# Kernel tuning notes

Measured on AMD Instinct MI355X. Metric: run time of the kernel, lower is better.

Reference implementation:

```python
import jax, jax.numpy as jnp
import numpy as np

D_MODEL = 768
N_HEADS = 12
D_K = D_MODEL // N_HEADS
NEG_INF = -1e9


def setup_inputs() -> dict:
    key = jax.random.key(0)
    ks = jax.random.split(key, 7)
    B, S = 4, 2048
    x = jax.random.normal(ks[0], (B, S, D_MODEL), dtype=jnp.float32)
    # causal mask, broadcastable to [B, H, S, S]
    mask = jnp.tril(jnp.ones((S, S), dtype=bool))[None, None, :, :]
    scale = 1.0 / np.sqrt(D_MODEL)
    Wq = jax.random.normal(ks[1], (D_MODEL, D_MODEL), dtype=jnp.float32) * scale
    bq = jnp.zeros((D_MODEL,), dtype=jnp.float32)
    Wk = jax.random.normal(ks[2], (D_MODEL, D_MODEL), dtype=jnp.float32) * scale
    bk = jnp.zeros((D_MODEL,), dtype=jnp.float32)
    Wv = jax.random.normal(ks[3], (D_MODEL, D_MODEL), dtype=jnp.float32) * scale
    bv = jnp.zeros((D_MODEL,), dtype=jnp.float32)
    return {"x": x, "mask": mask, "Wq": Wq, "bq": bq, "Wk": Wk, "bk": bk, "Wv": Wv, "bv": bv}


def reference(x, mask, Wq, bq, Wk, bk, Wv, bv):
    B, S, _ = x.shape
    # projections (torch Linear: y = x @ W.T + b)
    q = (x @ Wq.T + bq).reshape(B, S, N_HEADS, D_K)
    k = (x @ Wk.T + bk).reshape(B, S, N_HEADS, D_K)
    v = (x @ Wv.T + bv).reshape(B, S, N_HEADS, D_K)
    # scores: [B, H, S, S]
    scores = jnp.einsum("bqhd,bkhd->bhqk", q, k) / jnp.sqrt(jnp.float32(D_K))
    scores = jnp.where(mask, scores, NEG_INF)
    probs = jax.nn.softmax(scores, axis=-1)
    # attention: [B, H, S, D_K] -> [B, S, d_model]
    attn = jnp.einsum("bhqk,bkhd->bqhd", probs, v).reshape(B, S, D_MODEL)
    return attn
```

## Files before the change

kernel.cpp:

```cpp
#include <hip/hip_runtime.h>
#include <math.h>


#define S_LEN 2048
#define BATCH 4
#define HEADS 12
#define DM 768
#define DK 64
#define BH (BATCH*HEADS)
#define MROWS (BATCH*S_LEN)
#define QSCALE 0.1803368801111244f

typedef __attribute__((ext_vector_type(8))) short short8;
typedef __attribute__((ext_vector_type(4))) float floatx4;
typedef __attribute__((address_space(3))) unsigned char lds_byte;
typedef __attribute__((address_space(1))) const unsigned char glob_byte;

__device__ __forceinline__ unsigned short f2bf(float f) {
  union { float f; unsigned int u; } a; a.f = f;
  unsigned int u = a.u;
  return (unsigned short)((u + 0x7fffu + ((u >> 16) & 1u)) >> 16);
}
__device__ __forceinline__ unsigned short f2bf_rtz(float f) {
  union { float f; unsigned int u; } a; a.f = f;
  return (unsigned short)(a.u >> 16);
}

__global__ void cast_f32_bf16(const float* __restrict__ src,
                              unsigned short* __restrict__ dst, int n) {
  int i = (blockIdx.x * blockDim.x + threadIdx.x) * 4;
  if (i < n) {
    float4 v = *(const float4*)(src + i);
    ushort4 o;
    o.x = f2bf(v.x); o.y = f2bf(v.y); o.z = f2bf(v.z); o.w = f2bf(v.w);
    *(ushort4*)(dst + i) = o;
  }
}

__global__ void cast_w3(const float* __restrict__ w0, const float* __restrict__ w1,
                        const float* __restrict__ w2, unsigned short* __restrict__ dst,
                        int n) {
  const float* src = (blockIdx.y == 0) ? w0 : (blockIdx.y == 1) ? w1 : w2;
  int i = (blockIdx.x * blockDim.x + threadIdx.x) * 4;
  if (i < n) {
    float4 v = *(const float4*)(src + i);
    ushort4 o;
    o.x = f2bf(v.x); o.y = f2bf(v.y); o.z = f2bf(v.z); o.w = f2bf(v.w);
    *(ushort4*)(dst + (size_t)blockIdx.y * n + i) = o;
  }
}

__global__ __launch_bounds__(256) void qkv_gemm(
    const unsigned short* __restrict__ xb,
    const unsigned short* __restrict__ wb,
    const float* __restrict__ bq, const float* __restrict__ bk,
    const float* __restrict__ bv,
    unsigned short* __restrict__ qo,
    unsigned short* __restrict__ ko,
    unsigned short* __restrict__ vto) {
  __shared__ unsigned short a_lds[2 * 128 * 32];
  __shared__ unsigned short b_lds[2 * 128 * 32];
  const int mat = blockIdx.z;
  const int tid = threadIdx.x;
  const int wave = tid >> 6, lane = tid & 63, quad = lane >> 4, ln = lane & 15;
  const int wm = wave & 1, wn = wave >> 1;
  const int m_blk = blockIdx.x * 128, n_blk = blockIdx.y * 128;
  const unsigned short* w = wb + (size_t)mat * DM * DM;
  const int srow_i[2] = { (0 * 256 + wave * 64 + lane) >> 2,
                          (1 * 256 + wave * 64 + lane) >> 2 };
  const int sq = (lane & 3) * 8;

  const floatx4 fz = {0.f, 0.f, 0.f, 0.f};
  floatx4 acc[4][4];
#pragma unroll
  for (int mg = 0; mg < 4; mg++)
#pragma unroll
    for (int c = 0; c < 4; c++) acc[mg][c] = fz;

  for (int k0 = 0; k0 < DM; k0 += 64) {
#pragma unroll
    for (int p = 0; p < 2; p++)
#pragma unroll
      for (int i = 0; i < 2; i++) {
        const int cbase = i * 256 + wave * 64;
        const int row = srow_i[i];
        __builtin_amdgcn_global_load_lds(
            (glob_byte*)(xb + (size_t)(m_blk + row) * DM + k0 + p * 32 + sq),
            (lds_byte*)(a_lds + p * 4096 + cbase * 8), 16, 0, 0);
        __builtin_amdgcn_global_load_lds(
            (glob_byte*)(w + (size_t)(n_blk + row) * DM + k0 + p * 32 + sq),
            (lds_byte*)(b_lds + p * 4096 + cbase * 8), 16, 0, 0);
      }
    __syncthreads();

    short8 af[4][2], bf[4][2];
#pragma unroll
    for (int mg = 0; mg < 4; mg++)
#pragma unroll
      for (int p = 0; p < 2; p++)
        af[mg][p] = *(const short8*)(a_lds + p * 4096 + (wm * 64 + mg * 16 + ln) * 32 + quad * 8);
#pragma unroll
    for (int c = 0; c < 4; c++)
#pragma unroll
      for (int p = 0; p < 2; p++)
        bf[c][p] = *(const short8*)(b_lds + p * 4096 + (wn * 64 + c * 16 + ln) * 32 + quad * 8);
#pragma unroll
    for (int mg = 0; mg < 4; mg++)
#pragma unroll
      for (int c = 0; c < 4; c++) {
        acc[mg][c] = __builtin_amdgcn_mfma_f32_16x16x32_bf16(af[mg][0], bf[c][0], acc[mg][c], 0, 0, 0);
        acc[mg][c] = __builtin_amdgcn_mfma_f32_16x16x32_bf16(af[mg][1], bf[c][1], acc[mg][c], 0, 0, 0);
      }
    __syncthreads();
  }

  const float* bias = (mat == 0) ? bq : (mat == 1) ? bk : bv;
  const float oscale = (mat == 0) ? QSCALE : 1.0f;
  const int m_base = m_blk + wm * 64, n_base = n_blk + wn * 64;
#pragma unroll
  for (int mg = 0; mg < 4; mg++)
#pragma unroll
    for (int c = 0; c < 4; c++) {
      int gn = n_base + c * 16 + ln;
      int hd = gn >> 6, d = gn & 63;
      float bias_v = bias[gn] * oscale;
      int gm0 = m_base + mg * 16 + quad * 4;
      int bb = gm0 >> 11, s0 = gm0 & (S_LEN - 1);
      if (mat == 2) {
        ushort4 pk;
        pk.x = f2bf(acc[mg][c][0] + bias_v);
        pk.y = f2bf(acc[mg][c][1] + bias_v);
        pk.z = f2bf(acc[mg][c][2] + bias_v);
        pk.w = f2bf(acc[mg][c][3] + bias_v);
        *(ushort4*)(vto + (((size_t)(bb * HEADS + hd)) * DK + d) * S_LEN + s0) = pk;
      } else {
        unsigned short* dst = (mat == 0 ? qo : ko) +
            (((size_t)(bb * HEADS + hd)) * S_LEN + s0) * DK + d;
#pragma unroll
        for (int r = 0; r < 4; r++)
          dst[(size_t)r * DK] = f2bf(acc[mg][c][r] * oscale + bias_v);
      }
    }
}

__global__ __launch_bounds__(128) void flash_attn(
    const unsigned short* __restrict__ q,
    const unsigned short* __restrict__ k,
    const unsigned short* __restrict__ vt,
    float* __restrict__ out) {
  __shared__ unsigned short p_lds[2][32 * 64];
  const int id = blockIdx.x;
  const int bh = id % BH;
  const int qt = (S_LEN / 64 - 1) - (id / BH);
  const int q0 = qt * 64;
  const int tid = threadIdx.x;
  const int wave = tid >> 6, lane = tid & 63, quad = lane >> 4, ln = lane & 15;
  unsigned short* pl = p_lds[wave];
  const unsigned short* qp = q  + (size_t)bh * S_LEN * DK;
  const unsigned short* kp = k  + (size_t)bh * S_LEN * DK;
  const unsigned short* vp = vt + (size_t)bh * DK * S_LEN;
  const int qr_base = q0 + wave * 32;
  const floatx4 fz = {0.f, 0.f, 0.f, 0.f};

  unsigned short* wp[4];
#pragma unroll
  for (int kg = 0; kg < 4; kg++)
    wp[kg] = pl + quad * 256 + (((((kg ^ quad) & 3) << 1) | (ln >> 3)) * 8) + (ln & 7);
  const unsigned short* rp[2];
#pragma unroll
  for (int ss = 0; ss < 2; ss++)
    rp[ss] = pl + ln * 64 + (((ss * 4 + quad) ^ (((ln >> 2) & 3) << 1)) * 8);

  const int klane = ln * DK + quad * 8;
  const int vlane = ln * S_LEN + quad * 8;

  short8 ones;
#pragma unroll
  for (int j = 0; j < 8; j++) ones[j] = (short)0x3F80;

  short8 aq[2][2];
#pragma unroll
  for (int h = 0; h < 2; h++)
#pragma unroll
    for (int ss = 0; ss < 2; ss++)
      aq[h][ss] = *(const short8*)(qp + (qr_base + h * 16 + ln) * DK + ss * 32 + quad * 8);

  floatx4 o[2][4];
  floatx4 ol[2] = {fz, fz};
#pragma unroll
  for (int h = 0; h < 2; h++) {
    o[h][0] = fz; o[h][1] = fz; o[h][2] = fz; o[h][3] = fz;
  }

  auto loadK = [&](int k0, short8 (&kf)[4][2]) {
#pragma unroll
    for (int kg = 0; kg < 4; kg++)
#pragma unroll
      for (int ss = 0; ss < 2; ss++)
        kf[kg][ss] = *(const short8*)(kp + klane + (k0 + kg * 16) * DK + ss * 32);
  };

  auto body = [&](int k0, short8 (&kf)[4][2]) {
    short8 vf[4][2];
#pragma unroll
    for (int dg = 0; dg < 4; dg++)
#pragma unroll
      for (int ss = 0; ss < 2; ss++)
        vf[dg][ss] = *(const short8*)(vp + vlane + dg * 16 * S_LEN + k0 + ss * 32);
    const bool domask = (k0 + 63 > qr_base);
#pragma unroll
    for (int h = 0; h < 2; h++) {
      floatx4 sc[4];
#pragma unroll
      for (int kg = 0; kg < 4; kg++) {
        floatx4 tt = __builtin_amdgcn_mfma_f32_16x16x32_bf16(aq[h][0], kf[kg][0], fz, 0, 0, 0);
        sc[kg] = __builtin_amdgcn_mfma_f32_16x16x32_bf16(aq[h][1], kf[kg][1], tt, 0, 0, 0);
      }
#pragma unroll
      for (int kg = 0; kg < 4; kg++) {
        int key = k0 + kg * 16 + ln;
#pragma unroll
        for (int r = 0; r < 4; r++) {
          float pv = exp2f(sc[kg][r]);
          if (domask) {
            int qr = qr_base + h * 16 + quad * 4 + r;
            pv = (key <= qr) ? pv : 0.f;
          }
          wp[kg][h * 1024 + r * 64] = f2bf_rtz(pv);
        }
      }
      short8 ap0 = *(const short8*)(rp[0] + h * 1024);
      short8 ap1 = *(const short8*)(rp[1] + h * 1024);
#pragma unroll
      for (int dg = 0; dg < 4; dg++) {
        o[h][dg] = __builtin_amdgcn_mfma_f32_16x16x32_bf16(ap0, vf[dg][0], o[h][dg], 0, 0, 0);
        o[h][dg] = __builtin_amdgcn_mfma_f32_16x16x32_bf16(ap1, vf[dg][1], o[h][dg], 0, 0, 0);
      }
      ol[h] = __builtin_amdgcn_mfma_f32_16x16x32_bf16(ap0, ones, ol[h], 0, 0, 0);
      ol[h] = __builtin_amdgcn_mfma_f32_16x16x32_bf16(ap1, ones, ol[h], 0, 0, 0);
    }
  };

  const int kend = qr_base + 32;
  short8 kfa[4][2], kfb[4][2];
  loadK(0, kfa);
  int k0 = 0;
  for (; k0 + 64 < kend; k0 += 128) {
    loadK(k0 + 64, kfb);
    body(k0, kfa);
    loadK(k0 + 128, kfa);
    body(k0 + 64, kfb);
  }
  if (k0 < kend) body(k0, kfa);

  const int b = bh / HEADS, hd = bh % HEADS;
#pragma unroll
  for (int h = 0; h < 2; h++)
#pragma unroll
    for (int r = 0; r < 4; r++) {
      float inv = 1.f / ol[h][r];
      int qr = qr_base + h * 16 + quad * 4 + r;
      float* orow = out + ((size_t)(b * S_LEN + qr)) * DM + hd * DK;
      orow[ln]      = o[h][0][r] * inv;
      orow[16 + ln] = o[h][1][r] * inv;
      orow[32 + ln] = o[h][2][r] * inv;
      orow[48 + ln] = o[h][3][r] * inv;
    }
}

extern "C" void kernel_launch(void* const* d_in, const int* in_sizes, int n_in,
                              void* d_out, int out_size, void* d_ws, size_t ws_size,
                              hipStream_t stream) {
  const float* x  = (const float*)d_in[0];
  const float* Wq = (const float*)d_in[2];
  const float* bq = (const float*)d_in[3];
  const float* Wk = (const float*)d_in[4];
  const float* bk = (const float*)d_in[5];
  const float* Wv = (const float*)d_in[6];
  const float* bv = (const float*)d_in[7];
  float* out = (float*)d_out;

  const int NX = MROWS * DM;
  const int NW = DM * DM;
  unsigned short* xb = (unsigned short*)d_ws;
  unsigned short* wb = xb + NX;
  unsigned short* qo = wb + 3 * NW;
  unsigned short* ko = qo + (size_t)BH * S_LEN * DK;
  unsigned short* vt = ko + (size_t)BH * S_LEN * DK;

  cast_f32_bf16<<<(NX / 4 + 255) / 256, 256, 0, stream>>>(x, xb, NX);
  cast_w3<<<dim3((NW / 4 + 255) / 256, 3), 256, 0, stream>>>(Wq, Wk, Wv, wb, NW);

  qkv_gemm<<<dim3(MROWS / 128, DM / 128, 3), 256, 0, stream>>>(
      xb, wb, bq, bk, bv, qo, ko, vt);

  flash_attn<<<dim3((S_LEN / 64) * BH), 128, 0, stream>>>(qo, ko, vt, out);
}
```

Measured before the change: 254.3 us.

## Merge cast kernels and split attention into 128-key QK and PV phases

Merges the x and weight bf16 cast kernels into one launch, saving one kernel launch. In flash attention, the loop now computes QK^T and exp for two 64-key tiles into a larger per-wave LDS P buffer before running the PV MFMAs over all 128 keys. This replaces the explicit K double-buffering with a phase-split schedule. The goal is to batch more independent MFMA work and cut the number of per-tile switches between phases, at the cost of doubling LDS per block and dropping explicit K prefetch.

```diff
diff --git a/kernel.cpp b/kernel.cpp
--- a/kernel.cpp
+++ b/kernel.cpp
@@ -26,28 +26,29 @@
   return (unsigned short)(a.u >> 16);
 }
 
-__global__ void cast_f32_bf16(const float* __restrict__ src,
-                              unsigned short* __restrict__ dst, int n) {
-  int i = (blockIdx.x * blockDim.x + threadIdx.x) * 4;
-  if (i < n) {
-    float4 v = *(const float4*)(src + i);
-    ushort4 o;
-    o.x = f2bf(v.x); o.y = f2bf(v.y); o.z = f2bf(v.z); o.w = f2bf(v.w);
-    *(ushort4*)(dst + i) = o;
-  }
-}
-
-__global__ void cast_w3(const float* __restrict__ w0, const float* __restrict__ w1,
-                        const float* __restrict__ w2, unsigned short* __restrict__ dst,
-                        int n) {
-  const float* src = (blockIdx.y == 0) ? w0 : (blockIdx.y == 1) ? w1 : w2;
-  int i = (blockIdx.x * blockDim.x + threadIdx.x) * 4;
-  if (i < n) {
-    float4 v = *(const float4*)(src + i);
-    ushort4 o;
-    o.x = f2bf(v.x); o.y = f2bf(v.y); o.z = f2bf(v.z); o.w = f2bf(v.w);
-    *(ushort4*)(dst + (size_t)blockIdx.y * n + i) = o;
-  }
+__global__ void cast_all(const float* __restrict__ x,
+                         const float* __restrict__ w0, const float* __restrict__ w1,
+                         const float* __restrict__ w2,
+                         unsigned short* __restrict__ xb,
+                         unsigned short* __restrict__ wb) {
+  const int NXB = (MROWS * DM) / 1024;
+  const int NWB = (DM * DM) / 1024;
+  int id = blockIdx.x;
+  const float* src;
+  unsigned short* dst;
+  int blk;
+  if (id < NXB) { src = x; dst = xb; blk = id; }
+  else {
+    int t = id - NXB, m = t / NWB;
+    blk = t - m * NWB;
+    src = (m == 0) ? w0 : (m == 1) ? w1 : w2;
+    dst = wb + (size_t)m * (DM * DM);
+  }
+  int i = (blk * 256 + threadIdx.x) * 4;
+  float4 v = *(const float4*)(src + i);
+  ushort4 o;
+  o.x = f2bf(v.x); o.y = f2bf(v.y); o.z = f2bf(v.z); o.w = f2bf(v.w);
+  *(ushort4*)(dst + i) = o;
 }
 
 __global__ __launch_bounds__(256) void qkv_gemm(
@@ -148,7 +149,7 @@
     const unsigned short* __restrict__ k,
     const unsigned short* __restrict__ vt,
     float* __restrict__ out) {
-  __shared__ unsigned short p_lds[2][32 * 64];
+  __shared__ unsigned short p_lds[2][32 * 128];
   const int id = blockIdx.x;
   const int bh = id % BH;
   const int qt = (S_LEN / 64 - 1) - (id / BH);
@@ -162,14 +163,14 @@
   const int qr_base = q0 + wave * 32;
   const floatx4 fz = {0.f, 0.f, 0.f, 0.f};
 
-  unsigned short* wp[4];
-#pragma unroll
-  for (int kg = 0; kg < 4; kg++)
-    wp[kg] = pl + quad * 256 + (((((kg ^ quad) & 3) << 1) | (ln >> 3)) * 8) + (ln & 7);
-  const unsigned short* rp[2];
-#pragma unroll
-  for (int ss = 0; ss < 2; ss++)
-    rp[ss] = pl + ln * 64 + (((ss * 4 + quad) ^ (((ln >> 2) & 3) << 1)) * 8);
+  unsigned short* wp[8];
+#pragma unroll
+  for (int kg = 0; kg < 8; kg++)
+    wp[kg] = pl + quad * 512 + ((kg ^ quad) * 16) + ((ln >> 3) * 8) + (ln & 7);
+  const unsigned short* rp[4];
+#pragma unroll
+  for (int ss = 0; ss < 4; ss++)
+    rp[ss] = pl + ln * 128 + (((ss * 4 + quad) ^ (((ln >> 2) & 3) << 1)) * 8);
 
   const int klane = ln * DK + quad * 8;
   const int vlane = ln * S_LEN + quad * 8;
@@ -192,22 +193,14 @@
     o[h][0] = fz; o[h][1] = fz; o[h][2] = fz; o[h][3] = fz;
   }
 
-  auto loadK = [&](int k0, short8 (&kf)[4][2]) {
+  auto qk_phase = [&](int kbase, int kgbase) {
+    short8 kf[4][2];
 #pragma unroll
     for (int kg = 0; kg < 4; kg++)
 #pragma unroll
       for (int ss = 0; ss < 2; ss++)
-        kf[kg][ss] = *(const short8*)(kp + klane + (k0 + kg * 16) * DK + ss * 32);
-  };
-
-  auto body = [&](int k0, short8 (&kf)[4][2]) {
-    short8 vf[4][2];
-#pragma unroll
-    for (int dg = 0; dg < 4; dg++)
-#pragma unroll
-      for (int ss = 0; ss < 2; ss++)
-        vf[dg][ss] = *(const short8*)(vp + vlane + dg * 16 * S_LEN + k0 + ss * 32);
-    const bool domask = (k0 + 63 > qr_base);
+        kf[kg][ss] = *(const short8*)(kp + klane + (kbase + kg * 16) * DK + ss * 32);
+    const bool domask = (kbase + 63 > qr_base);
 #pragma unroll
     for (int h = 0; h < 2; h++) {
       floatx4 sc[4];
@@ -218,7 +211,7 @@
       }
 #pragma unroll
       for (int kg = 0; kg < 4; kg++) {
-        int key = k0 + kg * 16 + ln;
+        int key = kbase + kg * 16 + ln;
 #pragma unroll
         for (int r = 0; r < 4; r++) {
           float pv = exp2f(sc[kg][r]);
@@ -226,32 +219,40 @@
             int qr = qr_base + h * 16 + quad * 4 + r;
             pv = (key <= qr) ? pv : 0.f;
           }
-          wp[kg][h * 1024 + r * 64] = f2bf_rtz(pv);
+          wp[kgbase + kg][h * 2048 + r * 128] = f2bf_rtz(pv);
         }
       }
-      short8 ap0 = *(const short8*)(rp[0] + h * 1024);
-      short8 ap1 = *(const short8*)(rp[1] + h * 1024);
-#pragma unroll
-      for (int dg = 0; dg < 4; dg++) {
-        o[h][dg] = __builtin_amdgcn_mfma_f32_16x16x32_bf16(ap0, vf[dg][0], o[h][dg], 0, 0, 0);
-        o[h][dg] = __builtin_amdgcn_mfma_f32_16x16x32_bf16(ap1, vf[dg][1], o[h][dg], 0, 0, 0);
-      }
-      ol[h] = __builtin_amdgcn_mfma_f32_16x16x32_bf16(ap0, ones, ol[h], 0, 0, 0);
-      ol[h] = __builtin_amdgcn_mfma_f32_16x16x32_bf16(ap1, ones, ol[h], 0, 0, 0);
     }
   };
 
+  auto pv_phase = [&](int kbase, int nss) {
+    for (int ss = 0; ss < nss; ss++) {
+      short8 vf[4];
+#pragma unroll
+      for (int dg = 0; dg < 4; dg++)
+        vf[dg] = *(const short8*)(vp + vlane + dg * 16 * S_LEN + kbase + ss * 32);
+#pragma unroll
+      for (int h = 0; h < 2; h++) {
+        short8 ap = *(const short8*)(rp[ss] + h * 2048);
+#pragma unroll
+        for (int dg = 0; dg < 4; dg++)
+          o[h][dg] = __builtin_amdgcn_mfma_f32_16x16x32_bf16(ap, vf[dg], o[h][dg], 0, 0, 0);
+        ol[h] = __builtin_amdgcn_mfma_f32_16x16x32_bf16(ap, ones, ol[h], 0, 0, 0);
+      }
+    }
+  };
+
   const int kend = qr_base + 32;
-  short8 kfa[4][2], kfb[4][2];
-  loadK(0, kfa);
   int k0 = 0;
-  for (; k0 + 64 < kend; k0 += 128) {
-    loadK(k0 + 64, kfb);
-    body(k0, kfa);
-    loadK(k0 + 128, kfa);
-    body(k0 + 64, kfb);
-  }
-  if (k0 < kend) body(k0, kfa);
+  for (; k0 + 128 <= kend; k0 += 128) {
+    qk_phase(k0, 0);
+    qk_phase(k0 + 64, 4);
+    pv_phase(k0, 4);
+  }
+  for (; k0 < kend; k0 += 64) {
+    qk_phase(k0, 0);
+    pv_phase(k0, 2);
+  }
 
   const int b = bh / HEADS, hd = bh % HEADS;
 #pragma unroll
@@ -288,8 +289,8 @@
   unsigned short* ko = qo + (size_t)BH * S_LEN * DK;
   unsigned short* vt = ko + (size_t)BH * S_LEN * DK;
 
-  cast_f32_bf16<<<(NX / 4 + 255) / 256, 256, 0, stream>>>(x, xb, NX);
-  cast_w3<<<dim3((NW / 4 + 255) / 256, 3), 256, 0, stream>>>(Wq, Wk, Wv, wb, NW);
+  cast_all<<<dim3(NX / 1024 + 3 * (NW / 1024)), 256, 0, stream>>>(
+      x, Wq, Wk, Wv, xb, wb);
 
   qkv_gemm<<<dim3(MROWS / 128, DM / 128, 3), 256, 0, stream>>>(
       xb, wb, bq, bk, bv, qo, ko, vt);
```

After: 255.8 us. No clear change (+0.6%).
